# Kernel optimization log

Hardware: AMD Instinct MI355X
Metric: run time of the kernel (lower is better)

Reference implementation:

```python
import jax, jax.numpy as jnp
import numpy as np

N = 50000   # nodes
E = 500000  # edges (before self-loops)
H = 4       # heads
C = 128     # per-head channels
DIN = 182
D1 = H * C  # 512
LN_EPS = 1e-5
NEG_SLOPE = 0.2


def setup_inputs():
    key = jax.random.key(0)
    ks = jax.random.split(key, 26)
    def rn(k, shape, s=0.05):
        return jax.random.normal(k, shape, jnp.float32) * s
    return {
        'x': jax.random.normal(ks[0], (N, DIN), jnp.float32),
        'edge_index': jax.random.randint(ks[1], (2, E), 0, N, jnp.int32),
        # GAT layer 1 (182 -> 4x128)
        'W1': rn(ks[2], (DIN, D1)), 'as1': rn(ks[3], (H, C)), 'ad1': rn(ks[4], (H, C)), 'b1': rn(ks[5], (D1,)),
        # LayerNorm 1
        'g1': jnp.ones((D1,), jnp.float32), 'bn1': jnp.zeros((D1,), jnp.float32),
        # Expansion MLP 512->512->256
        'We1': rn(ks[6], (D1, D1)), 'bE1': rn(ks[7], (D1,)),
        'We2': rn(ks[8], (D1, 256)), 'bE2': rn(ks[9], (256,)),
        # Residual projection 512->256 + learned scale
        'Wr': rn(ks[10], (D1, 256)), 'br': rn(ks[11], (256,)),
        'rscale': jnp.float32(0.5),
        # GAT layer 2 (256 -> 4x128)
        'W2': rn(ks[12], (256, D1)), 'as2': rn(ks[13], (H, C)), 'ad2': rn(ks[14], (H, C)), 'b2': rn(ks[15], (D1,)),
        # LayerNorm 2
        'g2': jnp.ones((D1,), jnp.float32), 'bn2': jnp.zeros((D1,), jnp.float32),
        # Classifier 512->512->2
        'Wc1': rn(ks[16], (D1, D1)), 'bc1': rn(ks[17], (D1,)),
        'Wc2': rn(ks[18], (D1, 2)), 'bc2': rn(ks[19], (2,)),
    }


def layer_norm(x, g, b):
    mu = jnp.mean(x, axis=-1, keepdims=True)
    var = jnp.mean(jnp.square(x - mu), axis=-1, keepdims=True)
    return (x - mu) * jax.lax.rsqrt(var + LN_EPS) * g + b


def gat_conv(x, src, dst, W, a_src, a_dst, bias):
    # PyG GATConv (eval mode, self-loops already in src/dst), concat heads.
    h = (x @ W).reshape(N, H, C)                     # [N,H,C]
    al_s = jnp.sum(h * a_src, axis=-1)               # [N,H]
    al_d = jnp.sum(h * a_dst, axis=-1)               # [N,H]
    e = jax.nn.leaky_relu(al_s[src] + al_d[dst], NEG_SLOPE)  # [E',H]
    m = jax.ops.segment_max(e, dst, num_segments=N)  # segment softmax over target nbhd
    ex = jnp.exp(e - m[dst])
    denom = jax.ops.segment_sum(ex, dst, num_segments=N)
    alpha = ex / denom[dst]                          # [E',H]
    msg = h[src] * alpha[:, :, None]                 # [E',H,C]
    out = jax.ops.segment_sum(msg, dst, num_segments=N)
    return out.reshape(N, H * C) + bias


def reference(x, edge_index, W1, as1, ad1, b1, g1, bn1, We1, bE1, We2, bE2,
              Wr, br, rscale, W2, as2, ad2, b2, g2, bn2, Wc1, bc1, Wc2, bc2):
    loops = jnp.arange(N, dtype=edge_index.dtype)
    src = jnp.concatenate([edge_index[0], loops])    # add self-loops (PyG default)
    dst = jnp.concatenate([edge_index[1], loops])

    h1 = gat_conv(x, src, dst, W1, as1, ad1, b1)
    h1 = jax.nn.elu(layer_norm(h1, g1, bn1))
    h_exp = jax.nn.relu(h1 @ We1 + bE1) @ We2 + bE2  # expansion MLP (dropout=eval)
    h_comb = (h1 @ Wr + br) + rscale * h_exp         # residual combine

    h2 = gat_conv(h_comb, src, dst, W2, as2, ad2, b2)
    h2 = jax.nn.elu(layer_norm(h2, g2, bn2))
    out = jax.nn.relu(h2 @ Wc1 + bc1) @ Wc2 + bc2    # classifier -> [N,2]
    return out
```

## Files before the change

### kernel.cpp

```cpp
#include <hip/hip_runtime.h>
#include <hip/hip_bf16.h>
#include <math.h>

#define NNODES 50000
#define NEDGES 500000
#define NTOT   (NEDGES + NNODES)
#define MPAD   50048
#define D1     512
#define NH     4
#define LN_EPS 1e-5f
#define NEG_SLOPE 0.2f

#define SBLK 256
#define NSB  ((NNODES + SBLK - 1) / SBLK)

typedef __attribute__((ext_vector_type(8))) short short8;
typedef __attribute__((ext_vector_type(4))) float f32x4;
typedef __hip_bfloat16 bf16;

#define GLDS16(g, l) __builtin_amdgcn_global_load_lds( \
    (const __attribute__((address_space(1))) void*)(g), \
    (__attribute__((address_space(3))) void*)(l), 16, 0, 0)

__device__ __forceinline__ float bf2f(short u) {
    unsigned int x = ((unsigned int)(unsigned short)u) << 16;
    return __uint_as_float(x);
}
__device__ __forceinline__ short f2bf(float f) {
    unsigned int x = __float_as_uint(f);
    unsigned int r = (x + 0x7fffu + ((x >> 16) & 1u)) >> 16;
    return (short)r;
}
__device__ __forceinline__ float leaky(float e) {
    return (e >= 0.f) ? e : NEG_SLOPE * e;
}

__device__ __forceinline__ void xcd_map(int bid, int nwg, int ncolblk,
                                        int* p, int* c) {
    int q = nwg >> 3, r = nwg & 7;
    int xcd = bid & 7, j = bid >> 3;
    int w = (xcd < r) ? xcd * (q + 1) + j : r * (q + 1) + (xcd - r) * q + j;
    *p = w / ncolblk;
    *c = w - (*p) * ncolblk;
}


__global__ void k_count(const int* __restrict__ ei, int* __restrict__ counts) {
    int e = blockIdx.x * blockDim.x + threadIdx.x;
    if (e >= NTOT) return;
    int d = (e < NEDGES) ? ei[NEDGES + e] : (e - NEDGES);
    atomicAdd(&counts[d], 1);
}

__global__ void k_scan1(const int* __restrict__ counts, int* __restrict__ offs,
                        int* __restrict__ bsums) {
    __shared__ int s[SBLK];
    int tid = threadIdx.x, b = blockIdx.x;
    int idx = b * SBLK + tid;
    int v = (idx < NNODES) ? counts[idx] : 0;
    s[tid] = v;
    __syncthreads();
    for (int d = 1; d < SBLK; d <<= 1) {
        int t = (tid >= d) ? s[tid - d] : 0;
        __syncthreads();
        s[tid] += t;
        __syncthreads();
    }
    if (idx < NNODES) offs[idx] = s[tid] - v;
    if (tid == SBLK - 1) bsums[b] = s[tid];
}

__global__ void k_scan2(const int* __restrict__ bsums, int* __restrict__ bbase) {
    __shared__ int s[256];
    int tid = threadIdx.x;
    int v = (tid < NSB) ? bsums[tid] : 0;
    s[tid] = v;
    __syncthreads();
    for (int d = 1; d < 256; d <<= 1) {
        int t = (tid >= d) ? s[tid - d] : 0;
        __syncthreads();
        s[tid] += t;
        __syncthreads();
    }
    bbase[tid] = s[tid] - v;
    if (tid == 255) bbase[256] = s[255];
}

__global__ void k_scan3(int* __restrict__ offs, const int* __restrict__ bbase,
                        int* __restrict__ cursor) {
    int idx = blockIdx.x * 256 + threadIdx.x;
    if (idx < NNODES) {
        int v = offs[idx] + bbase[idx >> 8];
        offs[idx] = v;
        cursor[idx] = v;
    }
    if (idx == 0) offs[NNODES] = bbase[256];
}

__global__ void k_fill(const int* __restrict__ ei, int* __restrict__ cursor,
                       int* __restrict__ srcs) {
    int e = blockIdx.x * blockDim.x + threadIdx.x;
    if (e >= NTOT) return;
    int s, d;
    if (e < NEDGES) { s = ei[e]; d = ei[NEDGES + e]; }
    else            { s = d = e - NEDGES; }
    int pos = atomicAdd(&cursor[d], 1);
    srcs[pos] = s;
}


__global__ void k_wt_all(const float* __restrict__ W1, const float* __restrict__ We1,
                         const float* __restrict__ We2, const float* __restrict__ Wr,
                         const float* __restrict__ W2, const float* __restrict__ Wc1,
                         bf16* __restrict__ W1t, bf16* __restrict__ We1t,
                         bf16* __restrict__ We2t, bf16* __restrict__ Wrt,
                         bf16* __restrict__ W2t, bf16* __restrict__ Wc1t) {
    int which = blockIdx.y;
    const float* W; bf16* Wt; int K, N, Kpad;
    switch (which) {
        case 0:  W = W1;  Wt = W1t;  K = 182; N = 512; Kpad = 192; break;
        case 1:  W = We1; Wt = We1t; K = 512; N = 512; Kpad = 512; break;
        case 2:  W = We2; Wt = We2t; K = 512; N = 256; Kpad = 512; break;
        case 3:  W = Wr;  Wt = Wrt;  K = 512; N = 256; Kpad = 512; break;
        case 4:  W = W2;  Wt = W2t;  K = 256; N = 512; Kpad = 256; break;
        default: W = Wc1; Wt = Wc1t; K = 512; N = 512; Kpad = 512; break;
    }
    int idx = blockIdx.x * 256 + threadIdx.x;
    if (idx >= N * Kpad) return;
    int n = idx / Kpad, k = idx % Kpad;
    float v = (k < K) ? W[(size_t)k * N + n] : 0.f;
    Wt[idx] = __float2bfloat16(v);
}

__global__ void k_xconv(const float* __restrict__ x, bf16* __restrict__ xb) {
    int idx = blockIdx.x * 256 + threadIdx.x;
    if (idx >= MPAD * 192) return;
    int r = idx / 192, k = idx % 192;
    float v = (r < NNODES && k < 182) ? x[(size_t)r * 182 + k] : 0.f;
    xb[idx] = __float2bfloat16(v);
}


__global__ __launch_bounds__(256) void k_attn_logits(
        const bf16* __restrict__ h, const float* __restrict__ a_s,
        const float* __restrict__ a_d, float* __restrict__ als,
        float* __restrict__ ald) {
    int tid = threadIdx.x;
    int n = blockIdx.x * 4 + (tid >> 6);
    if (n >= NNODES) return;
    int lane = tid & 63;
    int ch0 = lane * 8;
    short8 hv = *reinterpret_cast<const short8*>(&h[(size_t)n * D1 + ch0]);
    float s1 = 0.f, s2 = 0.f;
    #pragma unroll
    for (int j = 0; j < 8; j++) {
        float v = bf2f(hv[j]);
        s1 += v * a_s[ch0 + j];
        s2 += v * a_d[ch0 + j];
    }
    #pragma unroll
    for (int o = 1; o < 16; o <<= 1) {
        s1 += __shfl_xor(s1, o);
        s2 += __shfl_xor(s2, o);
    }
    if ((lane & 15) == 0) {
        int head = lane >> 4;
        als[n * NH + head] = s1;
        ald[n * NH + head] = s2;
    }
}


__global__ __launch_bounds__(256) void k_edge_alpha(
        const float* __restrict__ als, const float* __restrict__ ald,
        const int* __restrict__ offs, const int* __restrict__ srcs,
        float* __restrict__ alpha) {
    int tid = threadIdx.x;
    int n = blockIdx.x * 4 + (tid >> 6);
    if (n >= NNODES) return;
    int lane = tid & 63;
    int head = lane >> 4, sub = lane & 15;
    int e0 = offs[n], e1 = offs[n + 1];
    float adh = ald[n * NH + head];

    float m = -1e30f;
    for (int k = e0 + sub; k < e1; k += 16)
        m = fmaxf(m, leaky(als[srcs[k] * NH + head] + adh));
    #pragma unroll
    for (int o = 1; o < 16; o <<= 1) m = fmaxf(m, __shfl_xor(m, o));
    float d = 0.f;
    for (int k = e0 + sub; k < e1; k += 16)
        d += __expf(leaky(als[srcs[k] * NH + head] + adh) - m);
    #pragma unroll
    for (int o = 1; o < 16; o <<= 1) d += __shfl_xor(d, o);
    float dinv = 1.f / d;
    for (int k = e0 + sub; k < e1; k += 16)
        alpha[k * NH + head] = __expf(leaky(als[srcs[k] * NH + head] + adh) - m) * dinv;
}


__global__ __launch_bounds__(256) void k_gat_aggregate(
        const bf16* __restrict__ h, const float* __restrict__ alpha,
        const int* __restrict__ offs, const int* __restrict__ srcs,
        const float* __restrict__ bias, const float* __restrict__ gamma,
        const float* __restrict__ beta, bf16* __restrict__ out) {
    int tid = threadIdx.x;
    int n = blockIdx.x * 4 + (tid >> 6);
    if (n >= NNODES) return;
    int lane = tid & 63;
    int head = lane >> 4;
    int ch0 = lane * 8;
    int e0 = offs[n], e1 = offs[n + 1];

    float acc[8] = {};
    for (int base = e0; base < e1; base += 64) {
        int cnt = min(64, e1 - base);
        int sv = (base + lane < e1) ? srcs[base + lane] : 0;
        int k = 0;
        for (; k + 8 <= cnt; k += 8) {
            int ss[8]; float pp[8]; short8 hh[8];
            #pragma unroll
            for (int u = 0; u < 8; u++) {
                ss[u] = __shfl(sv, k + u);
                pp[u] = alpha[(base + k + u) * NH + head];
            }
            #pragma unroll
            for (int u = 0; u < 8; u++)
                hh[u] = *reinterpret_cast<const short8*>(&h[(size_t)ss[u] * D1 + ch0]);
            #pragma unroll
            for (int j = 0; j < 8; j++) {
                float a = 0.f;
                #pragma unroll
                for (int u = 0; u < 8; u++) a += pp[u] * bf2f(hh[u][j]);
                acc[j] += a;
            }
        }
        for (; k + 4 <= cnt; k += 4) {
            int s0 = __shfl(sv, k),     s1 = __shfl(sv, k + 1);
            int s2 = __shfl(sv, k + 2), s3 = __shfl(sv, k + 3);
            float p0 = alpha[(base + k)     * NH + head];
            float p1 = alpha[(base + k + 1) * NH + head];
            float p2 = alpha[(base + k + 2) * NH + head];
            float p3 = alpha[(base + k + 3) * NH + head];
            short8 h0 = *reinterpret_cast<const short8*>(&h[(size_t)s0 * D1 + ch0]);
            short8 h1 = *reinterpret_cast<const short8*>(&h[(size_t)s1 * D1 + ch0]);
            short8 h2 = *reinterpret_cast<const short8*>(&h[(size_t)s2 * D1 + ch0]);
            short8 h3 = *reinterpret_cast<const short8*>(&h[(size_t)s3 * D1 + ch0]);
            #pragma unroll
            for (int j = 0; j < 8; j++)
                acc[j] += p0 * bf2f(h0[j]) + p1 * bf2f(h1[j])
                        + p2 * bf2f(h2[j]) + p3 * bf2f(h3[j]);
        }
        for (; k < cnt; k++) {
            int s0 = __shfl(sv, k);
            float p0 = alpha[(base + k) * NH + head];
            short8 h0 = *reinterpret_cast<const short8*>(&h[(size_t)s0 * D1 + ch0]);
            #pragma unroll
            for (int j = 0; j < 8; j++) acc[j] += p0 * bf2f(h0[j]);
        }
    }

    float v[8];
    float ps = 0.f;
    #pragma unroll
    for (int j = 0; j < 8; j++) { v[j] = acc[j] + bias[ch0 + j]; ps += v[j]; }
    #pragma unroll
    for (int o = 1; o < 64; o <<= 1) ps += __shfl_xor(ps, o);
    float mu = ps * (1.f / 512.f);
    float qs = 0.f;
    #pragma unroll
    for (int j = 0; j < 8; j++) { float dvj = v[j] - mu; qs += dvj * dvj; }
    #pragma unroll
    for (int o = 1; o < 64; o <<= 1) qs += __shfl_xor(qs, o);
    float rstd = rsqrtf(qs * (1.f / 512.f) + LN_EPS);

    short8 ov;
    #pragma unroll
    for (int j = 0; j < 8; j++) {
        float y = (v[j] - mu) * rstd * gamma[ch0 + j] + beta[ch0 + j];
        float e = (y > 0.f) ? y : (__expf(y) - 1.f);
        ov[j] = f2bf(e);
    }
    *reinterpret_cast<short8*>(&out[(size_t)n * D1 + ch0]) = ov;
}


#define EPI_BF       0
#define EPI_BRELU_BF 1
#define EPI_CLS      2

template<int EPI>
__global__ __launch_bounds__(256) void gemm64(
    const ushort* __restrict__ A, const ushort* __restrict__ Bt,
    const float* __restrict__ bias, bf16* __restrict__ Obf,
    float* __restrict__ Of32, const float* __restrict__ Wc2,
    int Mreal, int N, int K, const float* __restrict__ bc2, int ncolblk) {
    __shared__ __align__(16) ushort As[128 * 64];
    __shared__ __align__(16) ushort Bs[128 * 64];
    int tid = threadIdx.x;
    int wave = tid >> 6, lane = tid & 63;
    int pp, cc;
    xcd_map(blockIdx.x, gridDim.x, ncolblk, &pp, &cc);
    int brow = pp * 128;
    int bcol = cc * 128;
    int wm = (wave >> 1) * 64, wn = (wave & 1) * 64;
    int lr = lane & 15, hi = lane >> 4;
    int rx = lr & 7;
    int r8 = lane >> 3;
    int slotsw = (lane & 7) ^ r8;

    f32x4 acc[4][4] = {};

    for (int k0 = 0; k0 < K; k0 += 64) {
        if (k0) __syncthreads();
        #pragma unroll
        for (int i = 0; i < 4; i++) {
            int rb = wave * 32 + i * 8;
            GLDS16(A  + (size_t)(brow + rb + r8) * K + k0 + slotsw * 8, As + rb * 64);
            GLDS16(Bt + (size_t)(bcol + rb + r8) * K + k0 + slotsw * 8, Bs + rb * 64);
        }
        __syncthreads();

        #pragma unroll
        for (int sub = 0; sub < 2; sub++) {
            short8 af[4], bfr[4];
            int bsl = ((sub * 4 + hi) ^ rx) * 8;
            #pragma unroll
            for (int f = 0; f < 4; f++) {
                af[f]  = *reinterpret_cast<const short8*>(&As[(wm + f * 16 + lr) * 64 + bsl]);
                bfr[f] = *reinterpret_cast<const short8*>(&Bs[(wn + f * 16 + lr) * 64 + bsl]);
            }
            #pragma unroll
            for (int fm = 0; fm < 4; fm++)
                #pragma unroll
                for (int fn = 0; fn < 4; fn++)
                    acc[fm][fn] = __builtin_amdgcn_mfma_f32_16x16x32_bf16(
                        af[fm], bfr[fn], acc[fm][fn], 0, 0, 0);
        }
    }

    if (EPI == EPI_CLS) {
        float w2[4][2], b4[4];
        #pragma unroll
        for (int fn = 0; fn < 4; fn++) {
            int col = bcol + wn + fn * 16 + lr;
            w2[fn][0] = Wc2[col * 2];
            w2[fn][1] = Wc2[col * 2 + 1];
            b4[fn] = bias[col];
        }
        #pragma unroll
        for (int fm = 0; fm < 4; fm++) {
            #pragma unroll
            for (int r = 0; r < 4; r++) {
                int row = brow + wm + fm * 16 + hi * 4 + r;
                float s0 = 0.f, s1 = 0.f;
                #pragma unroll
                for (int fn = 0; fn < 4; fn++) {
                    float v = acc[fm][fn][r] + b4[fn];
                    v = v > 0.f ? v : 0.f;
                    s0 += v * w2[fn][0];
                    s1 += v * w2[fn][1];
                }
                #pragma unroll
                for (int o = 1; o < 16; o <<= 1) {
                    s0 += __shfl_xor(s0, o);
                    s1 += __shfl_xor(s1, o);
                }
                if (lr == 0 && row < Mreal) {
                    if (bcol == 0 && wn == 0) { s0 += bc2[0]; s1 += bc2[1]; }
                    atomicAdd(&Of32[row * 2],     s0);
                    atomicAdd(&Of32[row * 2 + 1], s1);
                }
            }
        }
        return;
    }

    #pragma unroll
    for (int fm = 0; fm < 4; fm++) {
        int row0 = brow + wm + fm * 16 + hi * 4;
        #pragma unroll
        for (int fn = 0; fn < 4; fn++) {
            int col = bcol + wn + fn * 16 + lr;
            #pragma unroll
            for (int r = 0; r < 4; r++) {
                int row = row0 + r;
                if (row >= Mreal) continue;
                float v = acc[fm][fn][r];
                if (EPI == EPI_BRELU_BF) { v += bias[col]; v = v > 0.f ? v : 0.f; }
                Obf[(size_t)row * N + col] = __float2bfloat16(v);
            }
        }
    }
}


__global__ __launch_bounds__(256) void gemm_dual64(
    const ushort* __restrict__ A1, const ushort* __restrict__ B1t,
    const ushort* __restrict__ A2, const ushort* __restrict__ B2t,
    const float* __restrict__ bias1, const float* __restrict__ bias2,
    bf16* __restrict__ Obf, int Mreal, int N, int K,
    const float* __restrict__ rsc, int ncolblk) {
    __shared__ __align__(16) ushort As[128 * 64];
    __shared__ __align__(16) ushort Bs[128 * 64];
    int tid = threadIdx.x;
    int wave = tid >> 6, lane = tid & 63;
    int pp, cc;
    xcd_map(blockIdx.x, gridDim.x, ncolblk, &pp, &cc);
    int brow = pp * 128;
    int bcol = cc * 128;
    int wm = (wave >> 1) * 64, wn = (wave & 1) * 64;
    int lr = lane & 15, hi = lane >> 4;
    int rx = lr & 7;
    int r8 = lane >> 3;
    int slotsw = (lane & 7) ^ r8;
    float rs = *rsc;

    f32x4 acc[4][4] = {};

    #pragma unroll
    for (int phase = 0; phase < 2; phase++) {
        const ushort* Ap = phase ? A2 : A1;
        const ushort* Bp = phase ? B2t : B1t;
        if (phase) {
            __syncthreads();
            #pragma unroll
            for (int fm = 0; fm < 4; fm++)
                #pragma unroll
                for (int fn = 0; fn < 4; fn++)
                    #pragma unroll
                    for (int r = 0; r < 4; r++) acc[fm][fn][r] *= rs;
        }
        for (int k0 = 0; k0 < K; k0 += 64) {
            if (k0 || phase) __syncthreads();
            #pragma unroll
            for (int i = 0; i < 4; i++) {
                int rb = wave * 32 + i * 8;
                GLDS16(Ap + (size_t)(brow + rb + r8) * K + k0 + slotsw * 8, As + rb * 64);
                GLDS16(Bp + (size_t)(bcol + rb + r8) * K + k0 + slotsw * 8, Bs + rb * 64);
            }
            __syncthreads();

            #pragma unroll
            for (int sub = 0; sub < 2; sub++) {
                short8 af[4], bfr[4];
                int bsl = ((sub * 4 + hi) ^ rx) * 8;
                #pragma unroll
                for (int f = 0; f < 4; f++) {
                    af[f]  = *reinterpret_cast<const short8*>(&As[(wm + f * 16 + lr) * 64 + bsl]);
                    bfr[f] = *reinterpret_cast<const short8*>(&Bs[(wn + f * 16 + lr) * 64 + bsl]);
                }
                #pragma unroll
                for (int fm = 0; fm < 4; fm++)
                    #pragma unroll
                    for (int fn = 0; fn < 4; fn++)
                        acc[fm][fn] = __builtin_amdgcn_mfma_f32_16x16x32_bf16(
                            af[fm], bfr[fn], acc[fm][fn], 0, 0, 0);
            }
        }
    }

    #pragma unroll
    for (int fm = 0; fm < 4; fm++) {
        int row0 = brow + wm + fm * 16 + hi * 4;
        #pragma unroll
        for (int fn = 0; fn < 4; fn++) {
            int col = bcol + wn + fn * 16 + lr;
            float be = bias2[col] + rs * bias1[col];
            #pragma unroll
            for (int r = 0; r < 4; r++) {
                int row = row0 + r;
                if (row >= Mreal) continue;
                Obf[(size_t)row * N + col] = __float2bfloat16(acc[fm][fn][r] + be);
            }
        }
    }
}


extern "C" void kernel_launch(void* const* d_in, const int* in_sizes, int n_in,
                              void* d_out, int out_size, void* d_ws, size_t ws_size,
                              hipStream_t stream) {
    const float* x   = (const float*)d_in[0];
    const int*   ei  = (const int*)d_in[1];
    const float* W1  = (const float*)d_in[2];
    const float* as1 = (const float*)d_in[3];
    const float* ad1 = (const float*)d_in[4];
    const float* b1  = (const float*)d_in[5];
    const float* g1  = (const float*)d_in[6];
    const float* bn1 = (const float*)d_in[7];
    const float* We1 = (const float*)d_in[8];
    const float* bE1 = (const float*)d_in[9];
    const float* We2 = (const float*)d_in[10];
    const float* bE2 = (const float*)d_in[11];
    const float* Wr  = (const float*)d_in[12];
    const float* br  = (const float*)d_in[13];
    const float* rsc = (const float*)d_in[14];
    const float* W2  = (const float*)d_in[15];
    const float* as2 = (const float*)d_in[16];
    const float* ad2 = (const float*)d_in[17];
    const float* b2  = (const float*)d_in[18];
    const float* g2  = (const float*)d_in[19];
    const float* bn2 = (const float*)d_in[20];
    const float* Wc1 = (const float*)d_in[21];
    const float* bc1 = (const float*)d_in[22];
    const float* Wc2 = (const float*)d_in[23];
    const float* bc2 = (const float*)d_in[24];
    float* out = (float*)d_out;

    char* ws = (char*)d_ws;
    size_t o = 0;
    auto alloc = [&](size_t bytes) { void* p = ws + o; o += (bytes + 255) & ~255ull; return p; };
    bf16* xb    = (bf16*)alloc((size_t)MPAD * 192 * 2);
    bf16* bufA  = (bf16*)alloc((size_t)MPAD * D1 * 2);
    bf16* bufB  = (bf16*)alloc((size_t)MPAD * D1 * 2);
    bf16* bufC  = (bf16*)alloc((size_t)MPAD * D1 * 2);
    bf16* hcb   = (bf16*)alloc((size_t)MPAD * 256 * 2);
    bf16* W1t   = (bf16*)alloc((size_t)512 * 192 * 2);
    bf16* We1t  = (bf16*)alloc((size_t)512 * 512 * 2);
    bf16* We2t  = (bf16*)alloc((size_t)256 * 512 * 2);
    bf16* Wrt   = (bf16*)alloc((size_t)256 * 512 * 2);
    bf16* W2t   = (bf16*)alloc((size_t)512 * 256 * 2);
    bf16* Wc1t  = (bf16*)alloc((size_t)512 * 512 * 2);
    float* als  = (float*)alloc((size_t)NNODES * NH * 4);
    float* ald  = (float*)alloc((size_t)NNODES * NH * 4);
    float* alpha= (float*)alloc((size_t)NTOT * NH * 4);
    int* counts = (int*)alloc((NNODES + 1) * 4);
    int* offs   = (int*)alloc((NNODES + 1) * 4);
    int* cursor = (int*)alloc((NNODES + 1) * 4);
    int* srcs   = (int*)alloc((size_t)NTOT * 4);
    int* bsums  = (int*)alloc((NSB + 1) * 4);
    int* bbase  = (int*)alloc(257 * 4);

    hipMemsetAsync(counts, 0, NNODES * 4, stream);
    k_count<<<(NTOT + 255) / 256, 256, 0, stream>>>(ei, counts);
    k_scan1<<<NSB, SBLK, 0, stream>>>(counts, offs, bsums);
    k_scan2<<<1, 256, 0, stream>>>(bsums, bbase);
    k_scan3<<<(NNODES + 255) / 256, 256, 0, stream>>>(offs, bbase, cursor);
    k_fill<<<(NTOT + 255) / 256, 256, 0, stream>>>(ei, cursor, srcs);

    k_wt_all<<<dim3(1024, 6), 256, 0, stream>>>(W1, We1, We2, Wr, W2, Wc1,
                                                W1t, We1t, We2t, Wrt, W2t, Wc1t);
    k_xconv<<<(MPAD * 192 + 255) / 256, 256, 0, stream>>>(x, xb);

    dim3 blk(256);
    int np = MPAD / 128;
    int g512 = np * 4, g256 = np * 2;
    int nwb = (NNODES + 3) / 4;

    gemm64<EPI_BF><<<g512, blk, 0, stream>>>((const ushort*)xb, (const ushort*)W1t,
        nullptr, bufA, nullptr, nullptr, NNODES, 512, 192, nullptr, 4);
    k_attn_logits<<<nwb, blk, 0, stream>>>(bufA, as1, ad1, als, ald);
    k_edge_alpha<<<nwb, blk, 0, stream>>>(als, ald, offs, srcs, alpha);
    k_gat_aggregate<<<nwb, blk, 0, stream>>>(bufA, alpha, offs, srcs, b1, g1, bn1, bufB);

    gemm64<EPI_BRELU_BF><<<g512, blk, 0, stream>>>((const ushort*)bufB, (const ushort*)We1t,
        bE1, bufC, nullptr, nullptr, NNODES, 512, 512, nullptr, 4);
    gemm_dual64<<<g256, blk, 0, stream>>>((const ushort*)bufC, (const ushort*)We2t,
        (const ushort*)bufB, (const ushort*)Wrt, bE2, br, hcb, NNODES, 256, 512, rsc, 2);

    gemm64<EPI_BF><<<g512, blk, 0, stream>>>((const ushort*)hcb, (const ushort*)W2t,
        nullptr, bufA, nullptr, nullptr, NNODES, 512, 256, nullptr, 4);
    k_attn_logits<<<nwb, blk, 0, stream>>>(bufA, as2, ad2, als, ald);
    k_edge_alpha<<<nwb, blk, 0, stream>>>(als, ald, offs, srcs, alpha);
    k_gat_aggregate<<<nwb, blk, 0, stream>>>(bufA, alpha, offs, srcs, b2, g2, bn2, bufB);

    hipMemsetAsync(out, 0, (size_t)out_size * 4, stream);
    gemm64<EPI_CLS><<<g512, blk, 0, stream>>>((const ushort*)bufB, (const ushort*)Wc1t,
        bc1, nullptr, out, Wc2, NNODES, 512, 512, bc2, 4);
}
```

Measured before the change: 510.5 us.

## Precompute W·a attention projections and compute logits from GEMM inputs

Attention logits are now computed from the narrow GEMM input (182/256 channels) using precomputed W·a_src and W·a_dst vectors, instead of re-reading the 512-wide bf16 GEMM output. This cuts the logits kernel's memory traffic and removes its dependence on the GEMM output. Separately, x-to-bf16 conversion now writes 8 elements per thread with vector stores. The logits use the full-precision projection rather than rounded bf16 h, which slightly changes numerics. The logits kernel also does more FMAs and 8 full-wave shuffle reductions per node.

Measured after the change: 607.4 us. +19.0%, slower.

```diff
diff --git a/kernel.cpp b/kernel.cpp
--- a/kernel.cpp
+++ b/kernel.cpp
@@ -134,39 +134,75 @@
 
 __global__ void k_xconv(const float* __restrict__ x, bf16* __restrict__ xb) {
     int idx = blockIdx.x * 256 + threadIdx.x;
-    if (idx >= MPAD * 192) return;
-    int r = idx / 192, k = idx % 192;
-    float v = (r < NNODES && k < 182) ? x[(size_t)r * 182 + k] : 0.f;
-    xb[idx] = __float2bfloat16(v);
-}
-
-
-__global__ __launch_bounds__(256) void k_attn_logits(
-        const bf16* __restrict__ h, const float* __restrict__ a_s,
-        const float* __restrict__ a_d, float* __restrict__ als,
-        float* __restrict__ ald) {
+    if (idx >= MPAD * 24) return;
+    int r = idx / 24, c8 = (idx % 24) * 8;
+    short8 ov;
+    #pragma unroll
+    for (int j = 0; j < 8; j++) {
+        int k = c8 + j;
+        float v = (r < NNODES && k < 182) ? x[(size_t)r * 182 + k] : 0.f;
+        ov[j] = f2bf(v);
+    }
+    *reinterpret_cast<short8*>(&xb[(size_t)r * 192 + c8]) = ov;
+}
+
+
+__global__ void k_wsd(const float* __restrict__ W1, const float* __restrict__ as1,
+                      const float* __restrict__ ad1, const float* __restrict__ W2,
+                      const float* __restrict__ as2, const float* __restrict__ ad2,
+                      float* __restrict__ wsd1, float* __restrict__ wsd2) {
+    int idx = blockIdx.x * 256 + threadIdx.x;
+    if (idx < 192 * 8) {
+        int k = idx >> 3, j = idx & 7;
+        int hh = j & 3;
+        float s = 0.f;
+        if (k < 182) {
+            const float* a = (j < 4) ? as1 : ad1;
+            for (int c = 0; c < 128; c++)
+                s += W1[(size_t)k * 512 + hh * 128 + c] * a[hh * 128 + c];
+        }
+        wsd1[idx] = s;
+    } else if (idx < 192 * 8 + 256 * 8) {
+        int i2 = idx - 192 * 8;
+        int k = i2 >> 3, j = i2 & 7;
+        int hh = j & 3;
+        const float* a = (j < 4) ? as2 : ad2;
+        float s = 0.f;
+        for (int c = 0; c < 128; c++)
+            s += W2[(size_t)k * 512 + hh * 128 + c] * a[hh * 128 + c];
+        wsd2[i2] = s;
+    }
+}
+
+
+__global__ __launch_bounds__(256) void k_logits_pre(
+        const bf16* __restrict__ A, const float* __restrict__ wsd,
+        float* __restrict__ als, float* __restrict__ ald, int K) {
     int tid = threadIdx.x;
     int n = blockIdx.x * 4 + (tid >> 6);
     if (n >= NNODES) return;
     int lane = tid & 63;
-    int ch0 = lane * 8;
-    short8 hv = *reinterpret_cast<const short8*>(&h[(size_t)n * D1 + ch0]);
-    float s1 = 0.f, s2 = 0.f;
-    #pragma unroll
-    for (int j = 0; j < 8; j++) {
-        float v = bf2f(hv[j]);
-        s1 += v * a_s[ch0 + j];
-        s2 += v * a_d[ch0 + j];
-    }
-    #pragma unroll
-    for (int o = 1; o < 16; o <<= 1) {
-        s1 += __shfl_xor(s1, o);
-        s2 += __shfl_xor(s2, o);
-    }
-    if ((lane & 15) == 0) {
-        int head = lane >> 4;
-        als[n * NH + head] = s1;
-        ald[n * NH + head] = s2;
+    int nch = K >> 3;
+    float p[8] = {};
+    if (lane < nch) {
+        short8 hv = *reinterpret_cast<const short8*>(&A[(size_t)n * K + lane * 8]);
+        #pragma unroll
+        for (int e = 0; e < 8; e++) {
+            float v = bf2f(hv[e]);
+            const float* w = &wsd[(lane * 8 + e) * 8];
+            #pragma unroll
+            for (int j = 0; j < 8; j++) p[j] += v * w[j];
+        }
+    }
+    #pragma unroll
+    for (int j = 0; j < 8; j++)
+        #pragma unroll
+        for (int o = 1; o < 64; o <<= 1) p[j] += __shfl_xor(p[j], o);
+    if (lane == 0) {
+        #pragma unroll
+        for (int j = 0; j < 4; j++) als[n * NH + j] = p[j];
+        #pragma unroll
+        for (int j = 0; j < 4; j++) ald[n * NH + j] = p[4 + j];
     }
 }
 
@@ -522,6 +558,8 @@
     bf16* Wrt   = (bf16*)alloc((size_t)256 * 512 * 2);
     bf16* W2t   = (bf16*)alloc((size_t)512 * 256 * 2);
     bf16* Wc1t  = (bf16*)alloc((size_t)512 * 512 * 2);
+    float* wsd1 = (float*)alloc(192 * 8 * 4);
+    float* wsd2 = (float*)alloc(256 * 8 * 4);
     float* als  = (float*)alloc((size_t)NNODES * NH * 4);
     float* ald  = (float*)alloc((size_t)NNODES * NH * 4);
     float* alpha= (float*)alloc((size_t)NTOT * NH * 4);
@@ -541,16 +579,17 @@
 
     k_wt_all<<<dim3(1024, 6), 256, 0, stream>>>(W1, We1, We2, Wr, W2, Wc1,
                                                 W1t, We1t, We2t, Wrt, W2t, Wc1t);
-    k_xconv<<<(MPAD * 192 + 255) / 256, 256, 0, stream>>>(x, xb);
+    k_xconv<<<(MPAD * 24 + 255) / 256, 256, 0, stream>>>(x, xb);
+    k_wsd<<<14, 256, 0, stream>>>(W1, as1, ad1, W2, as2, ad2, wsd1, wsd2);
 
     dim3 blk(256);
     int np = MPAD / 128;
     int g512 = np * 4, g256 = np * 2;
     int nwb = (NNODES + 3) / 4;
 
+    k_logits_pre<<<nwb, blk, 0, stream>>>(xb, wsd1, als, ald, 192);
     gemm64<EPI_BF><<<g512, blk, 0, stream>>>((const ushort*)xb, (const ushort*)W1t,
         nullptr, bufA, nullptr, nullptr, NNODES, 512, 192, nullptr, 4);
-    k_attn_logits<<<nwb, blk, 0, stream>>>(bufA, as1, ad1, als, ald);
     k_edge_alpha<<<nwb, blk, 0, stream>>>(als, ald, offs, srcs, alpha);
     k_gat_aggregate<<<nwb, blk, 0, stream>>>(bufA, alpha, offs, srcs, b1, g1, bn1, bufB);
 
@@ -559,9 +598,9 @@
     gemm_dual64<<<g256, blk, 0, stream>>>((const ushort*)bufC, (const ushort*)We2t,
         (const ushort*)bufB, (const ushort*)Wrt, bE2, br, hcb, NNODES, 256, 512, rsc, 2);
 
+    k_logits_pre<<<nwb, blk, 0, stream>>>(hcb, wsd2, als, ald, 256);
     gemm64<EPI_BF><<<g512, blk, 0, stream>>>((const ushort*)hcb, (const ushort*)W2t,
         nullptr, bufA, nullptr, nullptr, NNODES, 512, 256, nullptr, 4);
-    k_attn_logits<<<nwb, blk, 0, stream>>>(bufA, as2, ad2, als, ald);
     k_edge_alpha<<<nwb, blk, 0, stream>>>(als, ald, offs, srcs, alpha);
     k_gat_aggregate<<<nwb, blk, 0, stream>>>(bufA, alpha, offs, srcs, b2, g2, bn2, bufB);
 
```
